# Performance work log

Hardware: AMD Instinct MI355X
Metric: run time of the kernel (lower is better)

## Reference

```python
import jax, jax.numpy as jnp
import numpy as np

EMBED_DIM = 1024
NUM_HEADS = 16
HEAD_DIM = EMBED_DIM // NUM_HEADS


def setup_inputs() -> dict:
    key = jax.random.key(0)
    ks = jax.random.split(key, 5)
    s = 0.02
    return {
        "x": jax.random.normal(ks[0], (2, 2048, EMBED_DIM), dtype=jnp.float32),
        "w_qkv": jax.random.normal(ks[1], (EMBED_DIM, 3 * EMBED_DIM), dtype=jnp.float32) * s,
        "b_qkv": jnp.zeros((3 * EMBED_DIM,), dtype=jnp.float32),
        "w_out": jax.random.normal(ks[2], (EMBED_DIM, EMBED_DIM), dtype=jnp.float32) * s,
        "b_out": jnp.zeros((EMBED_DIM,), dtype=jnp.float32),
    }


def reference(x, w_qkv, b_qkv, w_out, b_out):
    B, T, C = x.shape
    qkv = x @ w_qkv + b_qkv                       # [B,T,3C]
    q, k, v = jnp.split(qkv, 3, axis=-1)
    # [B,T,C] -> [B,H,T,Dh]
    def heads(t):
        return t.reshape(B, T, NUM_HEADS, HEAD_DIM).transpose(0, 2, 1, 3)
    q, k, v = heads(q), heads(k), heads(v)
    scale = 1.0 / np.sqrt(HEAD_DIM).astype(np.float32)
    scores = jnp.einsum("bhqd,bhkd->bhqk", q, k) * scale  # [B,H,T,T]
    causal = jnp.tril(jnp.ones((T, T), dtype=bool))
    scores = jnp.where(causal[None, None], scores, -jnp.inf)
    attn = jax.nn.softmax(scores, axis=-1)
    out = jnp.einsum("bhqk,bhkd->bhqd", attn, v)  # [B,H,T,Dh]
    out = out.transpose(0, 2, 1, 3).reshape(B, T, C)
    return out @ w_out + b_out
```

## Files before the change

### kernel.cpp

```cpp
#include <hip/hip_runtime.h>

typedef unsigned short u16;
typedef unsigned int u32;
typedef __attribute__((ext_vector_type(8))) short bf16x8;
typedef __attribute__((ext_vector_type(4))) float f32x4;
typedef __attribute__((ext_vector_type(16))) float f32x16;

#define TOK   4096
#define EMB   1024
#define NQKV  3072
#define TSEQ  2048
#define NH    16

__device__ __forceinline__ u16 f2b(float f) {
  union { float f; unsigned u; } v; v.f = f;
  unsigned r = v.u + 0x7FFFu + ((v.u >> 16) & 1u);
  return (u16)(r >> 16);
}

__device__ __forceinline__ u32 pack_rn(float a, float b) {
  u32 ua = __float_as_uint(a) + 0x8000u;
  u32 ub = __float_as_uint(b) + 0x8000u;
  return __builtin_amdgcn_perm(ub, ua, 0x07060302u);
}

__device__ __forceinline__ f32x16 zero16() {
  f32x16 z;
#pragma unroll
  for (int i = 0; i < 16; i++) z[i] = 0.f;
  return z;
}


__global__ __launch_bounds__(256) void prep_kernel(const float* __restrict__ x,
                                                   u16* __restrict__ x_bf,
                                                   const float* __restrict__ w_qkv,
                                                   u16* __restrict__ wqkvT,
                                                   const float* __restrict__ w_out,
                                                   u16* __restrict__ woutT) {
  __shared__ u16 sm[64][65];
  int bid = blockIdx.x, tid = threadIdx.x;
  if (bid < 4096) {
    int i = bid * 256 + tid;
    float4 v = ((const float4*)x)[i];
    union { u16 us[4]; uint2 u2; } o;
    o.us[0] = f2b(v.x); o.us[1] = f2b(v.y); o.us[2] = f2b(v.z); o.us[3] = f2b(v.w);
    ((uint2*)x_bf)[i] = o.u2;
    return;
  }
  const float* src; u16* dst; int R, C, bx, by;
  if (bid < 4096 + 768) {
    int t = bid - 4096; bx = t % 48; by = t / 48;
    src = w_qkv; dst = wqkvT; R = EMB; C = NQKV;
  } else {
    int t = bid - 4096 - 768; bx = t & 15; by = t >> 4;
    src = w_out; dst = woutT; R = EMB; C = EMB;
  }
  int c0 = bx * 64, r0 = by * 64;
#pragma unroll
  for (int i = 0; i < 16; i++) {
    int idx = tid + i * 256;
    int r = idx >> 6, c = idx & 63;
    sm[r][c] = f2b(src[(size_t)(r0 + r) * C + c0 + c]);
  }
  __syncthreads();
#pragma unroll
  for (int i = 0; i < 16; i++) {
    int idx = tid + i * 256;
    int cc = idx >> 6, rr = idx & 63;
    dst[(size_t)(c0 + cc) * R + r0 + rr] = sm[rr][cc];
  }
}

__global__ __launch_bounds__(256) void transpose_v(const u16* __restrict__ V,
                                                   u16* __restrict__ Vt) {
  __shared__ u16 sm[64][72];
  int t0 = blockIdx.x * 64, bh = blockIdx.y;
  size_t base = (size_t)bh * TSEQ * 64;
  int tid = threadIdx.x;
  int r = tid >> 2, c = (tid & 3) * 16;
  *(bf16x8*)&sm[r][c]     = *(const bf16x8*)&V[base + (size_t)(t0 + r) * 64 + c];
  *(bf16x8*)&sm[r][c + 8] = *(const bf16x8*)&V[base + (size_t)(t0 + r) * 64 + c + 8];
  __syncthreads();
  int d = tid >> 2, tc = (tid & 3) * 16;
  union { u16 us[16]; uint4 v4[2]; } o;
#pragma unroll
  for (int i = 0; i < 16; i++) o.us[i] = sm[tc + i][d];
  *(uint4*)&Vt[base + (size_t)d * TSEQ + t0 + tc]     = o.v4[0];
  *(uint4*)&Vt[base + (size_t)d * TSEQ + t0 + tc + 8] = o.v4[1];
}


template <int MODE, int TM>
__global__ __launch_bounds__(256) void gemm_bt(const u16* __restrict__ A,
                                               const u16* __restrict__ Bt,
                                               const float* __restrict__ bias,
                                               u16* __restrict__ qb, u16* __restrict__ kb,
                                               u16* __restrict__ vb, float* __restrict__ outp,
                                               int K, int N) {
  constexpr int LDA = 68;
  constexpr int CT = (TM == 128) ? 4 : 2;
  constexpr int AC = TM / 32;
  __shared__ u16 As[TM][LDA];
  __shared__ u16 Bs[128][LDA];
  int tid = threadIdx.x;
  int m0 = blockIdx.y * TM, n0 = blockIdx.x * 128;
  int lane = tid & 63, wid = tid >> 6;
  int wm = (TM == 128) ? (wid >> 1) * 64 : 0;
  int wn = (TM == 128) ? (wid & 1) * 64 : wid * 32;
  int l15 = lane & 15, quad = lane >> 4;
  int lrow = lane >> 3, lcol = (lane & 7) * 8;

  f32x4 acc[4][CT];
#pragma unroll
  for (int i = 0; i < 4; i++)
#pragma unroll
    for (int j = 0; j < CT; j++) acc[i][j] = (f32x4){0.f, 0.f, 0.f, 0.f};

  bf16x8 ar[AC], br[4];
#pragma unroll
  for (int i = 0; i < AC; i++)
    ar[i] = *(const bf16x8*)&A[(size_t)(m0 + (wid * AC + i) * 8 + lrow) * K + lcol];
#pragma unroll
  for (int i = 0; i < 4; i++)
    br[i] = *(const bf16x8*)&Bt[(size_t)(n0 + (wid * 4 + i) * 8 + lrow) * K + lcol];

  for (int k0 = 0; k0 < K; k0 += 64) {
#pragma unroll
    for (int i = 0; i < AC; i++)
      *(bf16x8*)&As[(wid * AC + i) * 8 + lrow][lcol] = ar[i];
#pragma unroll
    for (int i = 0; i < 4; i++)
      *(bf16x8*)&Bs[(wid * 4 + i) * 8 + lrow][lcol] = br[i];
    __syncthreads();

    if (k0 + 64 < K) {
      int kn = k0 + 64;
#pragma unroll
      for (int i = 0; i < AC; i++)
        ar[i] = *(const bf16x8*)&A[(size_t)(m0 + (wid * AC + i) * 8 + lrow) * K + kn + lcol];
#pragma unroll
      for (int i = 0; i < 4; i++)
        br[i] = *(const bf16x8*)&Bt[(size_t)(n0 + (wid * 4 + i) * 8 + lrow) * K + kn + lcol];
    }

#pragma unroll
    for (int ks = 0; ks < 2; ks++) {
      bf16x8 af[4], bfr[CT];
#pragma unroll
      for (int rt = 0; rt < 4; rt++)
        af[rt] = *(const bf16x8*)&As[wm + rt * 16 + l15][ks * 32 + quad * 8];
#pragma unroll
      for (int ct = 0; ct < CT; ct++)
        bfr[ct] = *(const bf16x8*)&Bs[wn + ct * 16 + l15][ks * 32 + quad * 8];
#pragma unroll
      for (int rt = 0; rt < 4; rt++)
#pragma unroll
        for (int ct = 0; ct < CT; ct++)
          acc[rt][ct] = __builtin_amdgcn_mfma_f32_16x16x32_bf16(bfr[ct], af[rt], acc[rt][ct], 0, 0, 0);
    }
    __syncthreads();
  }

#pragma unroll
  for (int rt = 0; rt < 4; rt++) {
#pragma unroll
    for (int ct = 0; ct < CT; ct++) {
      int m = m0 + wm + rt * 16 + l15;
      int nb = n0 + wn + ct * 16 + quad * 4;
      float4 b4 = *(const float4*)&bias[nb];
      float v0 = acc[rt][ct][0] + b4.x, v1 = acc[rt][ct][1] + b4.y;
      float v2 = acc[rt][ct][2] + b4.z, v3 = acc[rt][ct][3] + b4.w;
      if (MODE == 0) {
        int sel = nb >> 10;
        int c = nb & 1023;
        int h = c >> 6, d0 = c & 63;
        int b = m >> 11, t = m & 2047;
        u16* dst = (sel == 0) ? qb : (sel == 1) ? kb : vb;
        union { u32 u[2]; uint2 u2; } o;
        o.u[0] = pack_rn(v0, v1);
        o.u[1] = pack_rn(v2, v3);
        *(uint2*)&dst[((((size_t)b * NH + h) * TSEQ + t) << 6) + d0] = o.u2;
      } else {
        float4 o = {v0, v1, v2, v3};
        *(float4*)&outp[(size_t)m * N + nb] = o;
      }
    }
  }
}


__global__ __launch_bounds__(256, 4) void attn_kernel(const u16* __restrict__ Qb,
                                                      const u16* __restrict__ Kb,
                                                      const u16* __restrict__ Vtb,
                                                      u16* __restrict__ O) {
  __shared__ u16 Ks[64][68];
  __shared__ u16 Vt[64][68];
  __shared__ float Cmb[2][16][64][2];
  __shared__ float Lmb[2][32];

  const float SCL = 0.18033688f;
  const float MOFF = 16.0f;

  int id = blockIdx.x;
  int bh = (id >> 5) & 31;
  int q5 = id & 31;
  int qt = ((id >> 8) & 1) ? (31 - q5) : q5;

  int tid = threadIdx.x, lane = tid & 63, w = tid >> 6;
  int sub = w & 1, par = w >> 1;
  int l31 = lane & 31, h = lane >> 5;
  const size_t hoff = (size_t)bh * TSEQ * 64;

  int qw = qt * 64 + sub * 32;
  int qg = qw + l31;

  bf16x8 qf[4];
  {
    const u16* qp = Qb + hoff + (size_t)qg * 64 + h * 8;
#pragma unroll
    for (int s = 0; s < 4; s++) qf[s] = *(const bf16x8*)(qp + s * 16);
  }

  f32x16 acc[2];
  acc[0] = zero16(); acc[1] = zero16();
  float l_i = 0.f;

  int r = tid >> 2, cb = (tid & 3) * 16;
  bf16x8 kr0, kr1, vr0, vr1;
  {
    const u16* kg = Kb + hoff + (size_t)r * 64 + cb;
    const u16* vg = Vtb + hoff + (size_t)r * TSEQ + cb;
    kr0 = *(const bf16x8*)kg;       kr1 = *(const bf16x8*)(kg + 8);
    vr0 = *(const bf16x8*)vg;       vr1 = *(const bf16x8*)(vg + 8);
  }

  for (int kt = 0; kt <= qt; kt++) {
    __syncthreads();
    *(bf16x8*)&Ks[r][cb]     = kr0;
    *(bf16x8*)&Ks[r][cb + 8] = kr1;
    *(bf16x8*)&Vt[r][cb]     = vr0;
    *(bf16x8*)&Vt[r][cb + 8] = vr1;
    __syncthreads();
    if (kt < qt) {
      const u16* kg = Kb + hoff + (size_t)((kt + 1) * 64 + r) * 64 + cb;
      const u16* vg = Vtb + hoff + (size_t)r * TSEQ + (kt + 1) * 64 + cb;
      kr0 = *(const bf16x8*)kg;     kr1 = *(const bf16x8*)(kg + 8);
      vr0 = *(const bf16x8*)vg;     vr1 = *(const bf16x8*)(vg + 8);
    }

    int kbt = kt * 64 + par * 32;
    if (kbt <= qw + 31) {
      f32x16 sacc = zero16();
#pragma unroll
      for (int s = 0; s < 4; s++) {
        bf16x8 kf = *(const bf16x8*)&Ks[par * 32 + l31][s * 16 + h * 8];
        sacc = __builtin_amdgcn_mfma_f32_32x32x16_bf16(kf, qf[s], sacc, 0, 0, 0);
      }

      if (kbt + 31 > qw) {
#pragma unroll
        for (int rr = 0; rr < 16; rr++) {
          int key = kbt + (rr & 3) + 8 * (rr >> 2) + 4 * h;
          if (key > qg) sacc[rr] = -1e30f;
        }
      }

#pragma unroll
      for (int rr = 0; rr < 16; rr++) {
        float p = exp2f(__builtin_fmaf(sacc[rr], SCL, -MOFF));
        sacc[rr] = p;
        l_i += p;
      }

#pragma unroll
      for (int s2 = 0; s2 < 2; s2++) {
        u32 u0 = pack_rn(sacc[8 * s2 + 0], sacc[8 * s2 + 1]);
        u32 u1 = pack_rn(sacc[8 * s2 + 2], sacc[8 * s2 + 3]);
        u32 u2 = pack_rn(sacc[8 * s2 + 4], sacc[8 * s2 + 5]);
        u32 u3 = pack_rn(sacc[8 * s2 + 6], sacc[8 * s2 + 7]);
        u32 s0 = h ? u0 : u2, s1 = h ? u1 : u3;
        u32 t0 = (u32)__shfl_xor((int)s0, 32);
        u32 t1 = (u32)__shfl_xor((int)s1, 32);
        union { u32 d[4]; bf16x8 v; } pf;
        pf.d[0] = h ? t0 : u0;
        pf.d[1] = h ? t1 : u1;
        pf.d[2] = h ? u2 : t0;
        pf.d[3] = h ? u3 : t1;
#pragma unroll
        for (int dt = 0; dt < 2; dt++) {
          bf16x8 vf = *(const bf16x8*)&Vt[dt * 32 + l31][par * 32 + s2 * 16 + h * 8];
          acc[dt] = __builtin_amdgcn_mfma_f32_32x32x16_bf16(vf, pf.v, acc[dt], 0, 0, 0);
        }
      }
    }
  }

  l_i += __shfl_xor(l_i, 32);

  __syncthreads();
  if (par == 1) {
#pragma unroll
    for (int dt = 0; dt < 2; dt++)
#pragma unroll
      for (int pr = 0; pr < 8; pr++) {
        Cmb[sub][dt * 8 + pr][lane][0] = acc[dt][2 * pr];
        Cmb[sub][dt * 8 + pr][lane][1] = acc[dt][2 * pr + 1];
      }
    if (h == 0) Lmb[sub][l31] = l_i;
  }
  __syncthreads();
  if (par == 0) {
#pragma unroll
    for (int dt = 0; dt < 2; dt++)
#pragma unroll
      for (int pr = 0; pr < 8; pr++) {
        acc[dt][2 * pr]     += Cmb[sub][dt * 8 + pr][lane][0];
        acc[dt][2 * pr + 1] += Cmb[sub][dt * 8 + pr][lane][1];
      }
    float lt = l_i + Lmb[sub][l31];
    float inv = 1.0f / lt;

    int b = bh >> 4, head = bh & 15;
    size_t rowbase = ((size_t)b * TSEQ + qg) * 1024 + head * 64;
#pragma unroll
    for (int dt = 0; dt < 2; dt++)
#pragma unroll
      for (int G = 0; G < 4; G++) {
        union { u32 u[2]; uint2 u2; } o;
        o.u[0] = pack_rn(acc[dt][4 * G + 0] * inv, acc[dt][4 * G + 1] * inv);
        o.u[1] = pack_rn(acc[dt][4 * G + 2] * inv, acc[dt][4 * G + 3] * inv);
        *(uint2*)&O[rowbase + dt * 32 + G * 8 + 4 * h] = o.u2;
      }
  }
}


extern "C" void kernel_launch(void* const* d_in, const int* in_sizes, int n_in,
                              void* d_out, int out_size, void* d_ws, size_t ws_size,
                              hipStream_t stream) {
  (void)in_sizes; (void)n_in; (void)out_size; (void)ws_size;
  const float* x     = (const float*)d_in[0];
  const float* w_qkv = (const float*)d_in[1];
  const float* b_qkv = (const float*)d_in[2];
  const float* w_out = (const float*)d_in[3];
  const float* b_out = (const float*)d_in[4];
  float* out = (float*)d_out;

  char* p = (char*)d_ws;
  u16* x_bf  = (u16*)p; p += (size_t)TOK * EMB * 2;
  u16* wqkvT = (u16*)p; p += (size_t)NQKV * EMB * 2;
  u16* woutT = (u16*)p; p += (size_t)EMB * EMB * 2;
  u16* Qb    = (u16*)p; p += (size_t)32 * TSEQ * 64 * 2;
  u16* Kb    = (u16*)p; p += (size_t)32 * TSEQ * 64 * 2;
  u16* Vraw  = (u16*)p; p += (size_t)32 * TSEQ * 64 * 2;
  u16* attn_o = (u16*)p;
  u16* Vtb   = x_bf;

  prep_kernel<<<dim3(4096 + 768 + 256), 256, 0, stream>>>(x, x_bf, w_qkv, wqkvT, w_out, woutT);
  gemm_bt<0, 128><<<dim3(NQKV / 128, TOK / 128), 256, 0, stream>>>(x_bf, wqkvT, b_qkv,
                                                                   Qb, Kb, Vraw, nullptr, EMB, NQKV);
  transpose_v<<<dim3(TSEQ / 64, 32), 256, 0, stream>>>(Vraw, Vtb);
  attn_kernel<<<dim3(1024), 256, 0, stream>>>(Qb, Kb, Vtb, attn_o);
  gemm_bt<1, 64><<<dim3(EMB / 128, TOK / 64), 256, 0, stream>>>(attn_o, woutT, b_out,
                                                                nullptr, nullptr, nullptr, out, EMB, EMB);
}
```

Baseline: 186.5 us.

## Double-buffer K/V tiles, pair causal query tiles per block, swizzle V layout

The attention kernel now processes two complementary causal query tiles (qt and 31-qt) per block, so each of 512 blocks does equal work. K/V tiles are double-buffered in shared memory, with one sync per iteration and a prefetch two tiles ahead. V is stored with an interleaved column order so the P fragment can be packed without cross-lane shuffles. Occupancy is lowered to 2 blocks per SM via launch bounds, and shared memory per block doubles.

After: 193.5 us. 3.7% more time.

```diff
diff --git a/kernel.cpp b/kernel.cpp
--- a/kernel.cpp
+++ b/kernel.cpp
@@ -190,12 +190,12 @@
 }
 
 
-__global__ __launch_bounds__(256, 4) void attn_kernel(const u16* __restrict__ Qb,
+__global__ __launch_bounds__(256, 2) void attn_kernel(const u16* __restrict__ Qb,
                                                       const u16* __restrict__ Kb,
                                                       const u16* __restrict__ Vtb,
                                                       u16* __restrict__ O) {
-  __shared__ u16 Ks[64][68];
-  __shared__ u16 Vt[64][68];
+  __shared__ u16 Ks[2][64][68];
+  __shared__ u16 Vt[2][64][68];
   __shared__ float Cmb[2][16][64][2];
   __shared__ float Lmb[2][32];
 
@@ -203,135 +203,152 @@
   const float MOFF = 16.0f;
 
   int id = blockIdx.x;
-  int bh = (id >> 5) & 31;
-  int q5 = id & 31;
-  int qt = ((id >> 8) & 1) ? (31 - q5) : q5;
+  int bh = id >> 4;
+  int p4 = id & 15;
 
   int tid = threadIdx.x, lane = tid & 63, w = tid >> 6;
   int sub = w & 1, par = w >> 1;
   int l31 = lane & 31, h = lane >> 5;
   const size_t hoff = (size_t)bh * TSEQ * 64;
 
-  int qw = qt * 64 + sub * 32;
-  int qg = qw + l31;
-
-  bf16x8 qf[4];
-  {
-    const u16* qp = Qb + hoff + (size_t)qg * 64 + h * 8;
-#pragma unroll
-    for (int s = 0; s < 4; s++) qf[s] = *(const bf16x8*)(qp + s * 16);
-  }
-
-  f32x16 acc[2];
-  acc[0] = zero16(); acc[1] = zero16();
-  float l_i = 0.f;
-
   int r = tid >> 2, cb = (tid & 3) * 16;
-  bf16x8 kr0, kr1, vr0, vr1;
-  {
-    const u16* kg = Kb + hoff + (size_t)r * 64 + cb;
-    const u16* vg = Vtb + hoff + (size_t)r * TSEQ + cb;
-    kr0 = *(const bf16x8*)kg;       kr1 = *(const bf16x8*)(kg + 8);
-    vr0 = *(const bf16x8*)vg;       vr1 = *(const bf16x8*)(vg + 8);
-  }
-
-  for (int kt = 0; kt <= qt; kt++) {
-    __syncthreads();
-    *(bf16x8*)&Ks[r][cb]     = kr0;
-    *(bf16x8*)&Ks[r][cb + 8] = kr1;
-    *(bf16x8*)&Vt[r][cb]     = vr0;
-    *(bf16x8*)&Vt[r][cb + 8] = vr1;
-    __syncthreads();
-    if (kt < qt) {
-      const u16* kg = Kb + hoff + (size_t)((kt + 1) * 64 + r) * 64 + cb;
-      const u16* vg = Vtb + hoff + (size_t)r * TSEQ + (kt + 1) * 64 + cb;
-      kr0 = *(const bf16x8*)kg;     kr1 = *(const bf16x8*)(kg + 8);
-      vr0 = *(const bf16x8*)vg;     vr1 = *(const bf16x8*)(vg + 8);
-    }
-
-    int kbt = kt * 64 + par * 32;
-    if (kbt <= qw + 31) {
-      f32x16 sacc = zero16();
-#pragma unroll
-      for (int s = 0; s < 4; s++) {
-        bf16x8 kf = *(const bf16x8*)&Ks[par * 32 + l31][s * 16 + h * 8];
-        sacc = __builtin_amdgcn_mfma_f32_32x32x16_bf16(kf, qf[s], sacc, 0, 0, 0);
+
+  for (int ph = 0; ph < 2; ph++) {
+    int qt = ph ? (31 - p4) : p4;
+    int qw = qt * 64 + sub * 32;
+    int qg = qw + l31;
+
+    bf16x8 qf[4];
+    {
+      const u16* qp = Qb + hoff + (size_t)qg * 64 + h * 8;
+#pragma unroll
+      for (int s = 0; s < 4; s++) qf[s] = *(const bf16x8*)(qp + s * 16);
+    }
+
+    f32x16 acc[2];
+    acc[0] = zero16(); acc[1] = zero16();
+    float l_i = 0.f;
+
+    bf16x8 kr0, kr1, vr0, vr1;
+    {
+      const u16* kg = Kb + hoff + (size_t)r * 64 + cb;
+      const u16* vg = Vtb + hoff + (size_t)r * TSEQ + cb;
+      bf16x8 k0 = *(const bf16x8*)kg, k1 = *(const bf16x8*)(kg + 8);
+      bf16x8 v0 = *(const bf16x8*)vg, v1 = *(const bf16x8*)(vg + 8);
+      *(bf16x8*)&Ks[0][r][cb]     = k0;
+      *(bf16x8*)&Ks[0][r][cb + 8] = k1;
+      union { bf16x8 v; uint2 d2[2]; u32 d[4]; } a0, a1;
+      a0.v = v0; a1.v = v1;
+      *(uint2*)&Vt[0][r][cb]      = (uint2){a0.d[0], a0.d[1]};
+      *(uint2*)&Vt[0][r][cb + 4]  = (uint2){a1.d[0], a1.d[1]};
+      *(uint2*)&Vt[0][r][cb + 8]  = (uint2){a0.d[2], a0.d[3]};
+      *(uint2*)&Vt[0][r][cb + 12] = (uint2){a1.d[2], a1.d[3]};
+    }
+    if (qt >= 1) {
+      const u16* kg = Kb + hoff + (size_t)(64 + r) * 64 + cb;
+      const u16* vg = Vtb + hoff + (size_t)r * TSEQ + 64 + cb;
+      kr0 = *(const bf16x8*)kg; kr1 = *(const bf16x8*)(kg + 8);
+      vr0 = *(const bf16x8*)vg; vr1 = *(const bf16x8*)(vg + 8);
+    }
+    __syncthreads();
+
+    for (int kt = 0; kt <= qt; kt++) {
+      int cur = kt & 1;
+      if (kt + 1 <= qt) {
+        int nxt = cur ^ 1;
+        *(bf16x8*)&Ks[nxt][r][cb]     = kr0;
+        *(bf16x8*)&Ks[nxt][r][cb + 8] = kr1;
+        union { bf16x8 v; u32 d[4]; } a0, a1;
+        a0.v = vr0; a1.v = vr1;
+        *(uint2*)&Vt[nxt][r][cb]      = (uint2){a0.d[0], a0.d[1]};
+        *(uint2*)&Vt[nxt][r][cb + 4]  = (uint2){a1.d[0], a1.d[1]};
+        *(uint2*)&Vt[nxt][r][cb + 8]  = (uint2){a0.d[2], a0.d[3]};
+        *(uint2*)&Vt[nxt][r][cb + 12] = (uint2){a1.d[2], a1.d[3]};
       }
-
-      if (kbt + 31 > qw) {
+      if (kt + 2 <= qt) {
+        const u16* kg = Kb + hoff + (size_t)((kt + 2) * 64 + r) * 64 + cb;
+        const u16* vg = Vtb + hoff + (size_t)r * TSEQ + (kt + 2) * 64 + cb;
+        kr0 = *(const bf16x8*)kg; kr1 = *(const bf16x8*)(kg + 8);
+        vr0 = *(const bf16x8*)vg; vr1 = *(const bf16x8*)(vg + 8);
+      }
+
+      int kbt = kt * 64 + par * 32;
+      if (kbt <= qw + 31) {
+        f32x16 sacc = zero16();
+#pragma unroll
+        for (int s = 0; s < 4; s++) {
+          bf16x8 kf = *(const bf16x8*)&Ks[cur][par * 32 + l31][s * 16 + h * 8];
+          sacc = __builtin_amdgcn_mfma_f32_32x32x16_bf16(kf, qf[s], sacc, 0, 0, 0);
+        }
+
+        if (kbt + 31 > qw) {
+#pragma unroll
+          for (int rr = 0; rr < 16; rr++) {
+            int key = kbt + (rr & 3) + 8 * (rr >> 2) + 4 * h;
+            if (key > qg) sacc[rr] = -1e30f;
+          }
+        }
+
 #pragma unroll
         for (int rr = 0; rr < 16; rr++) {
-          int key = kbt + (rr & 3) + 8 * (rr >> 2) + 4 * h;
-          if (key > qg) sacc[rr] = -1e30f;
+          float p = exp2f(__builtin_fmaf(sacc[rr], SCL, -MOFF));
+          sacc[rr] = p;
+          l_i += p;
+        }
+
+#pragma unroll
+        for (int s2 = 0; s2 < 2; s2++) {
+          union { u32 d[4]; bf16x8 v; } pf;
+#pragma unroll
+          for (int j = 0; j < 4; j++)
+            pf.d[j] = pack_rn(sacc[8 * s2 + 2 * j], sacc[8 * s2 + 2 * j + 1]);
+#pragma unroll
+          for (int dt = 0; dt < 2; dt++) {
+            bf16x8 vf = *(const bf16x8*)&Vt[cur][dt * 32 + l31][par * 32 + s2 * 16 + h * 8];
+            acc[dt] = __builtin_amdgcn_mfma_f32_32x32x16_bf16(vf, pf.v, acc[dt], 0, 0, 0);
+          }
         }
       }
-
-#pragma unroll
-      for (int rr = 0; rr < 16; rr++) {
-        float p = exp2f(__builtin_fmaf(sacc[rr], SCL, -MOFF));
-        sacc[rr] = p;
-        l_i += p;
-      }
-
-#pragma unroll
-      for (int s2 = 0; s2 < 2; s2++) {
-        u32 u0 = pack_rn(sacc[8 * s2 + 0], sacc[8 * s2 + 1]);
-        u32 u1 = pack_rn(sacc[8 * s2 + 2], sacc[8 * s2 + 3]);
-        u32 u2 = pack_rn(sacc[8 * s2 + 4], sacc[8 * s2 + 5]);
-        u32 u3 = pack_rn(sacc[8 * s2 + 6], sacc[8 * s2 + 7]);
-        u32 s0 = h ? u0 : u2, s1 = h ? u1 : u3;
-        u32 t0 = (u32)__shfl_xor((int)s0, 32);
-        u32 t1 = (u32)__shfl_xor((int)s1, 32);
-        union { u32 d[4]; bf16x8 v; } pf;
-        pf.d[0] = h ? t0 : u0;
-        pf.d[1] = h ? t1 : u1;
-        pf.d[2] = h ? u2 : t0;
-        pf.d[3] = h ? u3 : t1;
-#pragma unroll
-        for (int dt = 0; dt < 2; dt++) {
-          bf16x8 vf = *(const bf16x8*)&Vt[dt * 32 + l31][par * 32 + s2 * 16 + h * 8];
-          acc[dt] = __builtin_amdgcn_mfma_f32_32x32x16_bf16(vf, pf.v, acc[dt], 0, 0, 0);
-        }
-      }
-    }
-  }
-
-  l_i += __shfl_xor(l_i, 32);
-
-  __syncthreads();
-  if (par == 1) {
-#pragma unroll
-    for (int dt = 0; dt < 2; dt++)
-#pragma unroll
-      for (int pr = 0; pr < 8; pr++) {
-        Cmb[sub][dt * 8 + pr][lane][0] = acc[dt][2 * pr];
-        Cmb[sub][dt * 8 + pr][lane][1] = acc[dt][2 * pr + 1];
-      }
-    if (h == 0) Lmb[sub][l31] = l_i;
-  }
-  __syncthreads();
-  if (par == 0) {
-#pragma unroll
-    for (int dt = 0; dt < 2; dt++)
-#pragma unroll
-      for (int pr = 0; pr < 8; pr++) {
-        acc[dt][2 * pr]     += Cmb[sub][dt * 8 + pr][lane][0];
-        acc[dt][2 * pr + 1] += Cmb[sub][dt * 8 + pr][lane][1];
-      }
-    float lt = l_i + Lmb[sub][l31];
-    float inv = 1.0f / lt;
-
-    int b = bh >> 4, head = bh & 15;
-    size_t rowbase = ((size_t)b * TSEQ + qg) * 1024 + head * 64;
-#pragma unroll
-    for (int dt = 0; dt < 2; dt++)
-#pragma unroll
-      for (int G = 0; G < 4; G++) {
-        union { u32 u[2]; uint2 u2; } o;
-        o.u[0] = pack_rn(acc[dt][4 * G + 0] * inv, acc[dt][4 * G + 1] * inv);
-        o.u[1] = pack_rn(acc[dt][4 * G + 2] * inv, acc[dt][4 * G + 3] * inv);
-        *(uint2*)&O[rowbase + dt * 32 + G * 8 + 4 * h] = o.u2;
-      }
+      __syncthreads();
+    }
+
+    l_i += __shfl_xor(l_i, 32);
+
+    if (par == 1) {
+#pragma unroll
+      for (int dt = 0; dt < 2; dt++)
+#pragma unroll
+        for (int pr = 0; pr < 8; pr++) {
+          Cmb[sub][dt * 8 + pr][lane][0] = acc[dt][2 * pr];
+          Cmb[sub][dt * 8 + pr][lane][1] = acc[dt][2 * pr + 1];
+        }
+      if (h == 0) Lmb[sub][l31] = l_i;
+    }
+    __syncthreads();
+    if (par == 0) {
+#pragma unroll
+      for (int dt = 0; dt < 2; dt++)
+#pragma unroll
+        for (int pr = 0; pr < 8; pr++) {
+          acc[dt][2 * pr]     += Cmb[sub][dt * 8 + pr][lane][0];
+          acc[dt][2 * pr + 1] += Cmb[sub][dt * 8 + pr][lane][1];
+        }
+      float lt = l_i + Lmb[sub][l31];
+      float inv = 1.0f / lt;
+
+      int b = bh >> 4, head = bh & 15;
+      size_t rowbase = ((size_t)b * TSEQ + qg) * 1024 + head * 64;
+#pragma unroll
+      for (int dt = 0; dt < 2; dt++)
+#pragma unroll
+        for (int G = 0; G < 4; G++) {
+          union { u32 u[2]; uint2 u2; } o;
+          o.u[0] = pack_rn(acc[dt][4 * G + 0] * inv, acc[dt][4 * G + 1] * inv);
+          o.u[1] = pack_rn(acc[dt][4 * G + 2] * inv, acc[dt][4 * G + 3] * inv);
+          *(uint2*)&O[rowbase + dt * 32 + G * 8 + 4 * h] = o.u2;
+        }
+    }
+    __syncthreads();
   }
 }
 
@@ -361,7 +378,7 @@
   gemm_bt<0, 128><<<dim3(NQKV / 128, TOK / 128), 256, 0, stream>>>(x_bf, wqkvT, b_qkv,
                                                                    Qb, Kb, Vraw, nullptr, EMB, NQKV);
   transpose_v<<<dim3(TSEQ / 64, 32), 256, 0, stream>>>(Vraw, Vtb);
-  attn_kernel<<<dim3(1024), 256, 0, stream>>>(Qb, Kb, Vtb, attn_o);
+  attn_kernel<<<dim3(512), 256, 0, stream>>>(Qb, Kb, Vtb, attn_o);
   gemm_bt<1, 64><<<dim3(EMB / 128, TOK / 64), 256, 0, stream>>>(attn_o, woutT, b_out,
                                                                 nullptr, nullptr, nullptr, out, EMB, EMB);
 }
```

## Use direct global-to-LDS loads with XOR swizzle; permute V layout to drop shuffles

Applied to the files above, without the earlier changes.

The GEMM now loads A and B tiles straight from global memory into LDS with global_load_lds, and uses an XOR-swizzled unpadded layout in place of padding to avoid bank conflicts. This removes the register staging, but it also drops the register prefetch of the next K tile, so loads no longer overlap with compute. In attention, V is written to LDS in an interleaved order so that the packed P fragments line up with the V fragments without cross-lane shuffles. This removes two shfl_xor per sub-step, at the cost of narrower LDS stores.

After: 193.4 us. 3.7% more time.

```diff
diff --git a/kernel.cpp b/kernel.cpp
--- a/kernel.cpp
+++ b/kernel.cpp
@@ -29,6 +29,11 @@
 #pragma unroll
   for (int i = 0; i < 16; i++) z[i] = 0.f;
   return z;
+}
+
+__device__ __forceinline__ void gload_lds16(const u16* g, u16* l) {
+  __builtin_amdgcn_global_load_lds((const __attribute__((address_space(1))) void*)g,
+                                   (__attribute__((address_space(3))) void*)l, 16, 0, 0);
 }
 
 
@@ -98,18 +103,17 @@
                                                u16* __restrict__ qb, u16* __restrict__ kb,
                                                u16* __restrict__ vb, float* __restrict__ outp,
                                                int K, int N) {
-  constexpr int LDA = 68;
   constexpr int CT = (TM == 128) ? 4 : 2;
   constexpr int AC = TM / 32;
-  __shared__ u16 As[TM][LDA];
-  __shared__ u16 Bs[128][LDA];
+  __shared__ u16 As[TM][64];
+  __shared__ u16 Bs[128][64];
   int tid = threadIdx.x;
   int m0 = blockIdx.y * TM, n0 = blockIdx.x * 128;
   int lane = tid & 63, wid = tid >> 6;
   int wm = (TM == 128) ? (wid >> 1) * 64 : 0;
   int wn = (TM == 128) ? (wid & 1) * 64 : wid * 32;
   int l15 = lane & 15, quad = lane >> 4;
-  int lrow = lane >> 3, lcol = (lane & 7) * 8;
+  int lrow = lane >> 3, lc8 = lane & 7;
 
   f32x4 acc[4][CT];
 #pragma unroll
@@ -117,42 +121,36 @@
 #pragma unroll
     for (int j = 0; j < CT; j++) acc[i][j] = (f32x4){0.f, 0.f, 0.f, 0.f};
 
-  bf16x8 ar[AC], br[4];
-#pragma unroll
-  for (int i = 0; i < AC; i++)
-    ar[i] = *(const bf16x8*)&A[(size_t)(m0 + (wid * AC + i) * 8 + lrow) * K + lcol];
-#pragma unroll
-  for (int i = 0; i < 4; i++)
-    br[i] = *(const bf16x8*)&Bt[(size_t)(n0 + (wid * 4 + i) * 8 + lrow) * K + lcol];
-
   for (int k0 = 0; k0 < K; k0 += 64) {
 #pragma unroll
-    for (int i = 0; i < AC; i++)
-      *(bf16x8*)&As[(wid * AC + i) * 8 + lrow][lcol] = ar[i];
-#pragma unroll
-    for (int i = 0; i < 4; i++)
-      *(bf16x8*)&Bs[(wid * 4 + i) * 8 + lrow][lcol] = br[i];
+    for (int i = 0; i < AC; i++) {
+      int chunk = wid * AC + i;
+      int row = chunk * 8 + lrow;
+      int src = 8 * (lc8 ^ (row & 7));
+      gload_lds16(&A[(size_t)(m0 + row) * K + k0 + src], &As[chunk * 8][0]);
+    }
+#pragma unroll
+    for (int i = 0; i < 4; i++) {
+      int chunk = wid * 4 + i;
+      int row = chunk * 8 + lrow;
+      int src = 8 * (lc8 ^ (row & 7));
+      gload_lds16(&Bt[(size_t)(n0 + row) * K + k0 + src], &Bs[chunk * 8][0]);
+    }
     __syncthreads();
-
-    if (k0 + 64 < K) {
-      int kn = k0 + 64;
-#pragma unroll
-      for (int i = 0; i < AC; i++)
-        ar[i] = *(const bf16x8*)&A[(size_t)(m0 + (wid * AC + i) * 8 + lrow) * K + kn + lcol];
-#pragma unroll
-      for (int i = 0; i < 4; i++)
-        br[i] = *(const bf16x8*)&Bt[(size_t)(n0 + (wid * 4 + i) * 8 + lrow) * K + kn + lcol];
-    }
 
 #pragma unroll
     for (int ks = 0; ks < 2; ks++) {
       bf16x8 af[4], bfr[CT];
 #pragma unroll
-      for (int rt = 0; rt < 4; rt++)
-        af[rt] = *(const bf16x8*)&As[wm + rt * 16 + l15][ks * 32 + quad * 8];
-#pragma unroll
-      for (int ct = 0; ct < CT; ct++)
-        bfr[ct] = *(const bf16x8*)&Bs[wn + ct * 16 + l15][ks * 32 + quad * 8];
+      for (int rt = 0; rt < 4; rt++) {
+        int row = wm + rt * 16 + l15;
+        af[rt] = *(const bf16x8*)&As[row][8 * ((ks * 4 + quad) ^ (row & 7))];
+      }
+#pragma unroll
+      for (int ct = 0; ct < CT; ct++) {
+        int row = wn + ct * 16 + l15;
+        bfr[ct] = *(const bf16x8*)&Bs[row][8 * ((ks * 4 + quad) ^ (row & 7))];
+      }
 #pragma unroll
       for (int rt = 0; rt < 4; rt++)
 #pragma unroll
@@ -239,8 +237,14 @@
     __syncthreads();
     *(bf16x8*)&Ks[r][cb]     = kr0;
     *(bf16x8*)&Ks[r][cb + 8] = kr1;
-    *(bf16x8*)&Vt[r][cb]     = vr0;
-    *(bf16x8*)&Vt[r][cb + 8] = vr1;
+    {
+      union { bf16x8 v; u32 d[4]; } a0, a1;
+      a0.v = vr0; a1.v = vr1;
+      *(uint2*)&Vt[r][cb]      = (uint2){a0.d[0], a0.d[1]};
+      *(uint2*)&Vt[r][cb + 4]  = (uint2){a1.d[0], a1.d[1]};
+      *(uint2*)&Vt[r][cb + 8]  = (uint2){a0.d[2], a0.d[3]};
+      *(uint2*)&Vt[r][cb + 12] = (uint2){a1.d[2], a1.d[3]};
+    }
     __syncthreads();
     if (kt < qt) {
       const u16* kg = Kb + hoff + (size_t)((kt + 1) * 64 + r) * 64 + cb;
@@ -275,18 +279,10 @@
 
 #pragma unroll
       for (int s2 = 0; s2 < 2; s2++) {
-        u32 u0 = pack_rn(sacc[8 * s2 + 0], sacc[8 * s2 + 1]);
-        u32 u1 = pack_rn(sacc[8 * s2 + 2], sacc[8 * s2 + 3]);
-        u32 u2 = pack_rn(sacc[8 * s2 + 4], sacc[8 * s2 + 5]);
-        u32 u3 = pack_rn(sacc[8 * s2 + 6], sacc[8 * s2 + 7]);
-        u32 s0 = h ? u0 : u2, s1 = h ? u1 : u3;
-        u32 t0 = (u32)__shfl_xor((int)s0, 32);
-        u32 t1 = (u32)__shfl_xor((int)s1, 32);
         union { u32 d[4]; bf16x8 v; } pf;
-        pf.d[0] = h ? t0 : u0;
-        pf.d[1] = h ? t1 : u1;
-        pf.d[2] = h ? u2 : t0;
-        pf.d[3] = h ? u3 : t1;
+#pragma unroll
+        for (int j = 0; j < 4; j++)
+          pf.d[j] = pack_rn(sacc[8 * s2 + 2 * j], sacc[8 * s2 + 2 * j + 1]);
 #pragma unroll
         for (int dt = 0; dt < 2; dt++) {
           bf16x8 vf = *(const bf16x8*)&Vt[dt * 32 + l31][par * 32 + s2 * 16 + h * 8];
```
